# Performance work log

Hardware: AMD Instinct MI355X
Metric: run time of the kernel (lower is better)

The kernel has to match this reference:

```python
import jax, jax.numpy as jnp
import numpy as np

D_MODEL = 768
H = 12
D_FF = 3072
EPS = 1e-6


def _layernorm(x, alpha, bias):
    # torch.std default is Bessel-corrected (ddof=1); denom is (std + eps)
    mean = jnp.mean(x, axis=-1, keepdims=True)
    var = jnp.sum((x - mean) ** 2, axis=-1, keepdims=True) / (x.shape[-1] - 1)
    std = jnp.sqrt(var)
    return alpha * (x - mean) / (std + EPS) + bias


def _linear(x, w, b):
    # torch nn.Linear: y = x @ W.T + b, W is [out, in]
    return jnp.einsum('...i,oi->...o', x, w) + b


def setup_inputs() -> dict:
    key = jax.random.key(0)
    ks = jax.random.split(key, 16)
    B, S = 8, 1024
    sc = 1.0 / np.sqrt(D_MODEL)
    inp = {
        'x': jax.random.normal(ks[0], (B, S, D_MODEL), dtype=jnp.float32),
        'mask': jax.random.randint(ks[1], (B, 1, 1, S), 0, 2, dtype=jnp.int32),
        'wq': jax.random.normal(ks[2], (D_MODEL, D_MODEL), dtype=jnp.float32) * sc,
        'bq': jnp.zeros((D_MODEL,), jnp.float32),
        'wk': jax.random.normal(ks[3], (D_MODEL, D_MODEL), dtype=jnp.float32) * sc,
        'bk': jnp.zeros((D_MODEL,), jnp.float32),
        'wv': jax.random.normal(ks[4], (D_MODEL, D_MODEL), dtype=jnp.float32) * sc,
        'bv': jnp.zeros((D_MODEL,), jnp.float32),
        'wo': jax.random.normal(ks[5], (D_MODEL, D_MODEL), dtype=jnp.float32) * sc,
        'bo': jnp.zeros((D_MODEL,), jnp.float32),
        'ln1_a': jnp.ones((D_MODEL,), jnp.float32),
        'ln1_b': jnp.zeros((D_MODEL,), jnp.float32),
        'ln2_a': jnp.ones((D_MODEL,), jnp.float32),
        'ln2_b': jnp.zeros((D_MODEL,), jnp.float32),
        'w1': jax.random.normal(ks[6], (D_FF, D_MODEL), dtype=jnp.float32) * sc,
        'b1': jnp.zeros((D_FF,), jnp.float32),
        'w2': jax.random.normal(ks[7], (D_MODEL, D_FF), dtype=jnp.float32) * (1.0 / np.sqrt(D_FF)),
        'b2': jnp.zeros((D_MODEL,), jnp.float32),
    }
    return inp


def reference(x, mask, wq, bq, wk, bk, wv, bv, wo, bo,
              ln1_a, ln1_b, ln2_a, ln2_b, w1, b1, w2, b2):
    B, S, _ = x.shape
    d_k = D_MODEL // H

    # --- residual 1: pre-LN self-attention (dropout identity at eval) ---
    xn = _layernorm(x, ln1_a, ln1_b)
    q = _linear(xn, wq, bq).reshape(B, S, H, d_k).transpose(0, 2, 1, 3)
    k = _linear(xn, wk, bk).reshape(B, S, H, d_k).transpose(0, 2, 1, 3)
    v = _linear(xn, wv, bv).reshape(B, S, H, d_k).transpose(0, 2, 1, 3)

    scores = jnp.einsum('bhqd,bhkd->bhqk', q, k) / jnp.sqrt(jnp.float32(d_k))
    # faithful quirk: masked positions set to 1e-9, NOT -inf
    scores = jnp.where(mask == 0, jnp.float32(1e-9), scores)
    attn = jax.nn.softmax(scores, axis=-1)
    ctx = jnp.einsum('bhqk,bhkd->bhqd', attn, v)
    ctx = ctx.transpose(0, 2, 1, 3).reshape(B, S, D_MODEL)
    x = x + _linear(ctx, wo, bo)

    # --- residual 2: pre-LN feed-forward ---
    xn = _layernorm(x, ln2_a, ln2_b)
    ff = _linear(jax.nn.relu(_linear(xn, w1, b1)), w2, b2)
    return x + ff
```

## Files before the change

### kernel.cpp

```cpp
#include <hip/hip_runtime.h>
#include <stdint.h>

#define D_MODEL 768
#define D_FF    3072
#define NH      12
#define DK      64
#define BB      8
#define SS      1024
#define NTOK    (BB*SS)
#define QST     2304

typedef float          f32x4  __attribute__((ext_vector_type(4)));
typedef __bf16         bf16x8 __attribute__((ext_vector_type(8)));
typedef unsigned short us8v   __attribute__((ext_vector_type(8)));
typedef unsigned short us4v   __attribute__((ext_vector_type(4)));

__device__ __forceinline__ unsigned short f2b(float f) {
  unsigned int u = __builtin_bit_cast(unsigned int, f);
  u = (u + 0x7fffu + ((u >> 16) & 1u)) >> 16;
  return (unsigned short)u;
}
__device__ __forceinline__ float b2f(unsigned short h) {
  unsigned int u = ((unsigned int)h) << 16;
  return __builtin_bit_cast(float, u);
}
__device__ __forceinline__ float exp2a(float x) {
  float r; asm("v_exp_f32 %0, %1" : "=v"(r) : "v"(x)); return r;
}
__device__ __forceinline__ unsigned int cvtpk(float lo, float hi) {
  unsigned int r;
  asm("v_cvt_pk_bf16_f32 %0, %1, %2" : "=v"(r) : "v"(lo), "v"(hi));
  return r;
}

#define N4TOT 1769472
__global__ __launch_bounds__(256) void cast6_kernel(
    const float* __restrict__ s0, const float* __restrict__ s1,
    const float* __restrict__ s2, const float* __restrict__ s3,
    const float* __restrict__ s4, const float* __restrict__ s5,
    unsigned short* __restrict__ d0, unsigned short* __restrict__ d1,
    unsigned short* __restrict__ d2, unsigned short* __restrict__ d3,
    unsigned short* __restrict__ d4, unsigned short* __restrict__ d5) {
  int i = blockIdx.x * 256 + threadIdx.x;
  if (i >= N4TOT) return;
  const float* src; unsigned short* dst; int off;
  if (i < 147456)       { src = s0; dst = d0; off = i; }
  else if (i < 294912)  { src = s1; dst = d1; off = i - 147456; }
  else if (i < 442368)  { src = s2; dst = d2; off = i - 294912; }
  else if (i < 589824)  { src = s3; dst = d3; off = i - 442368; }
  else if (i < 1179648) { src = s4; dst = d4; off = i - 589824; }
  else                  { src = s5; dst = d5; off = i - 1179648; }
  float4 f = ((const float4*)src)[off];
  us4v o; o.x = f2b(f.x); o.y = f2b(f.y); o.z = f2b(f.z); o.w = f2b(f.w);
  *(us4v*)(dst + (size_t)off * 4) = o;
}

__global__ __launch_bounds__(256) void ln_kernel(const float* __restrict__ x,
                                                 const float* __restrict__ ga,
                                                 const float* __restrict__ gb,
                                                 unsigned short* __restrict__ y) {
  int row = blockIdx.x;
  const float* xr = x + (size_t)row * D_MODEL;
  int t = threadIdx.x, w = t >> 6, l = t & 63;
  float v0 = xr[t], v1 = xr[t + 256], v2 = xr[t + 512];
  float s = v0 + v1 + v2;
  #pragma unroll
  for (int off = 32; off; off >>= 1) s += __shfl_xor(s, off);
  __shared__ float red[4];
  __shared__ float stats[2];
  if (l == 0) red[w] = s;
  __syncthreads();
  if (t == 0) stats[0] = (red[0] + red[1] + red[2] + red[3]) * (1.0f / 768.0f);
  __syncthreads();
  float mean = stats[0];
  float d0 = v0 - mean, d1 = v1 - mean, d2 = v2 - mean;
  float ss = d0 * d0 + d1 * d1 + d2 * d2;
  #pragma unroll
  for (int off = 32; off; off >>= 1) ss += __shfl_xor(ss, off);
  __syncthreads();
  if (l == 0) red[w] = ss;
  __syncthreads();
  if (t == 0) {
    float tot = red[0] + red[1] + red[2] + red[3];
    stats[1] = 1.0f / (sqrtf(tot * (1.0f / 767.0f)) + 1e-6f);
  }
  __syncthreads();
  float inv = stats[1];
  unsigned short* yr = y + (size_t)row * D_MODEL;
  yr[t]       = f2b(ga[t]       * (d0 * inv) + gb[t]);
  yr[t + 256] = f2b(ga[t + 256] * (d1 * inv) + gb[t + 256]);
  yr[t + 512] = f2b(ga[t + 512] * (d2 * inv) + gb[t + 512]);
}

#define GLDS(g, l) __builtin_amdgcn_global_load_lds( \
    (__attribute__((address_space(1))) const void*)(g), \
    (__attribute__((address_space(3))) void*)(l), 16, 0, 0)

template<int BN>
__global__ __launch_bounds__(256) void gemm_t(
    const unsigned short* __restrict__ A,
    const unsigned short* __restrict__ W,
    const float* __restrict__ biasA,
    const float* __restrict__ biasB,
    const float* __restrict__ biasC,
    int segw,
    const float* __restrict__ resid,
    float* __restrict__ outF,
    unsigned short* __restrict__ outB,
    int M, int N, int K, int relu) {
  constexpr int BK  = (BN == 128) ? 32 : 64;
  constexpr int WC  = (BN == 128) ? 2 : 1;
  constexpr int MF  = (BN == 128) ? 4 : 2;
  constexpr int NF  = 4;
  constexpr int ASZ = 128 * BK;
  constexpr int BSZ = BN * BK;
  __shared__ unsigned short As[2 * ASZ];
  __shared__ unsigned short Bs[2 * BSZ];
  int t = threadIdx.x;
  int w = t >> 6, l = t & 63;
  int brow = blockIdx.x * 128;
  int bcol = blockIdx.y * BN;
  int wr = (w / WC) * (MF * 16);
  int wc = (w % WC) * (NF * 16);

  const unsigned short *ga0, *ga1, *gb0, *gb1;
  if constexpr (BN == 128) {
    ga0 = A + (size_t)(brow + (t >> 2)) * K + (t & 3) * 8;
    ga1 = ga0 + (size_t)64 * K;
    gb0 = W + (size_t)(bcol + (t >> 2)) * K + (t & 3) * 8;
    gb1 = gb0 + (size_t)64 * K;
  } else {
    int r5 = t >> 3;
    int swz = (t & 7) ^ (r5 & 7);
    ga0 = A + (size_t)(brow + r5) * K + swz * 8;
    gb0 = W + (size_t)(bcol + r5) * K + swz * 8;
    ga1 = gb1 = nullptr;
  }

  f32x4 acc[MF][NF];
  #pragma unroll
  for (int m = 0; m < MF; m++)
    #pragma unroll
    for (int n = 0; n < NF; n++)
      acc[m][n] = (f32x4){0.f, 0.f, 0.f, 0.f};

  int arow = wr + (l & 15);
  int bcw  = wc + (l & 15);
  int g    = l >> 4;
  int kk   = g * 8;
  const int nt = K / BK;

  auto stage = [&](int ti, int buf) {
    int k0 = ti * BK;
    if constexpr (BN == 128) {
      GLDS(ga0 + k0, As + buf * ASZ + t * 8);
      GLDS(ga1 + k0, As + buf * ASZ + 2048 + t * 8);
      GLDS(gb0 + k0, Bs + buf * BSZ + t * 8);
      GLDS(gb1 + k0, Bs + buf * BSZ + 2048 + t * 8);
    } else {
      #pragma unroll
      for (int i = 0; i < 4; i++)
        GLDS(ga0 + k0 + (size_t)(32 * i) * K, As + buf * ASZ + i * 2048 + t * 8);
      #pragma unroll
      for (int i = 0; i < 2; i++)
        GLDS(gb0 + k0 + (size_t)(32 * i) * K, Bs + buf * BSZ + i * 2048 + t * 8);
    }
  };

  stage(0, 0);
  __syncthreads();

  int cb = 0;
  for (int ti = 0; ti < nt; ti++) {
    if (ti + 1 < nt) stage(ti + 1, cb ^ 1);
    #pragma unroll
    for (int h = 0; h < BK / 32; h++) {
      bf16x8 af[MF], bfv[NF];
      #pragma unroll
      for (int m = 0; m < MF; m++) {
        int aro = arow + m * 16;
        if constexpr (BN == 128)
          af[m] = *(const bf16x8*)(As + cb * ASZ + aro * 32 + kk);
        else
          af[m] = *(const bf16x8*)(As + cb * ASZ + aro * 64 +
                                   ((((h << 2) + g) ^ (l & 7)) << 3));
      }
      #pragma unroll
      for (int n = 0; n < NF; n++) {
        int bco = bcw + n * 16;
        if constexpr (BN == 128)
          bfv[n] = *(const bf16x8*)(Bs + cb * BSZ + bco * 32 + kk);
        else
          bfv[n] = *(const bf16x8*)(Bs + cb * BSZ + bco * 64 +
                                    ((((h << 2) + g) ^ (l & 7)) << 3));
      }
      #pragma unroll
      for (int m = 0; m < MF; m++)
        #pragma unroll
        for (int n = 0; n < NF; n++)
          acc[m][n] = __builtin_amdgcn_mfma_f32_16x16x32_bf16(af[m], bfv[n], acc[m][n], 0, 0, 0);
    }
    if (ti + 1 < nt) __syncthreads();
    cb ^= 1;
  }

  #pragma unroll
  for (int n = 0; n < NF; n++) {
    int col = bcol + wc + n * 16 + (l & 15);
    int seg = col / segw, off = col - seg * segw;
    const float* bp = (seg == 0) ? biasA : ((seg == 1) ? biasB : biasC);
    float bv = bp[off];
    #pragma unroll
    for (int m = 0; m < MF; m++) {
      int row0 = brow + wr + m * 16 + (l >> 4) * 4;
      #pragma unroll
      for (int r = 0; r < 4; r++) {
        int row = row0 + r;
        float vacc = acc[m][n][r] + bv;
        if (resid) vacc += resid[(size_t)row * N + col];
        if (relu)  vacc = fmaxf(vacc, 0.f);
        if (outF)  outF[(size_t)row * N + col] = vacc;
        if (outB)  outB[(size_t)row * N + col] = f2b(vacc);
      }
    }
  }
}

#define PPAD 72
#define KPAD 72
#define SM_C1 0.18033688011112043f
#define SM_C2 1.4426950408889634e-9f

__global__ __launch_bounds__(256) void attn_mfma(
    const unsigned short* __restrict__ qkv,
    const int* __restrict__ mask,
    unsigned short* __restrict__ ctx) {
  int bh = blockIdx.x;
  int qt = blockIdx.y;
  int b = bh / NH, h = bh % NH;
  int t = threadIdx.x, w = t >> 6, l = t & 63;
  int ql = l & 15, g = l >> 4;

  const unsigned short* kp = qkv + 768 + h * DK;
  const unsigned short* vp = qkv + 1536 + h * DK;

  __shared__ unsigned short Ks[2][4096];
  __shared__ unsigned short Vt[64 * KPAD];
  __shared__ unsigned short Ps[128 * PPAD];
  __shared__ float mk01[64];

  int srow = t >> 3;
  int sblk = t & 7;
  int sb0  = sblk ^ (srow & 7);
  int sb1  = sblk ^ ((srow + 32) & 7);

  bf16x8 qf[2][2];
  {
    const unsigned short* qp = qkv + h * DK;
    size_t row0 = (size_t)(b * SS + qt * 128 + w * 32 + ql);
    #pragma unroll
    for (int s = 0; s < 2; s++)
      #pragma unroll
      for (int ks = 0; ks < 2; ks++)
        qf[s][ks] = *(const bf16x8*)(qp + (row0 + s * 16) * QST + ks * 32 + g * 8);
  }

  {
    size_t tok0 = (size_t)(b * SS);
    GLDS(kp + (tok0 + srow) * QST + sb0 * 8, &Ks[0][t * 8]);
    GLDS(kp + (tok0 + srow + 32) * QST + sb1 * 8, &Ks[0][2048 + t * 8]);
  }
  us8v vA, vB;
  {
    const unsigned short* vs = vp + ((size_t)(b * SS) + l) * QST + w * 16;
    vA = *(const us8v*)vs;
    vB = *(const us8v*)(vs + 8);
  }
  float mkreg = mask[b * SS + (t & 63)] ? 1.0f : 0.0f;

  f32x4 acc_o[2][4];
  #pragma unroll
  for (int s = 0; s < 2; s++)
    #pragma unroll
    for (int nf = 0; nf < 4; nf++) acc_o[s][nf] = (f32x4){0.f, 0.f, 0.f, 0.f};
  float mrun[2] = {-INFINITY, -INFINITY};
  float lrun[2] = {0.f, 0.f};

  int cur = 0;
  for (int kt = 0; kt < 16; kt++) {
    #pragma unroll
    for (int j = 0; j < 8; j++) {
      Vt[(w * 16 + j)     * KPAD + l] = vA[j];
      Vt[(w * 16 + 8 + j) * KPAD + l] = vB[j];
    }
    if (t < 64) mk01[t] = mkreg;
    __syncthreads();

    if (kt + 1 < 16) {
      size_t tn = (size_t)(b * SS + (kt + 1) * 64);
      GLDS(kp + (tn + srow) * QST + sb0 * 8, &Ks[cur ^ 1][t * 8]);
      GLDS(kp + (tn + srow + 32) * QST + sb1 * 8, &Ks[cur ^ 1][2048 + t * 8]);
      const unsigned short* vs2 = vp + (tn + l) * QST + w * 16;
      vA = *(const us8v*)vs2;
      vB = *(const us8v*)(vs2 + 8);
      mkreg = mask[b * SS + (kt + 1) * 64 + (t & 63)] ? 1.0f : 0.0f;
    }

    f32x4 sa[2][4];
    #pragma unroll
    for (int s = 0; s < 2; s++)
      #pragma unroll
      for (int kf = 0; kf < 4; kf++) sa[s][kf] = (f32x4){0.f, 0.f, 0.f, 0.f};
    #pragma unroll
    for (int ks = 0; ks < 2; ks++) {
      bf16x8 kfr[4];
      #pragma unroll
      for (int kf = 0; kf < 4; kf++) {
        int row = kf * 16 + ql;
        kfr[kf] = *(const bf16x8*)(&Ks[cur][row * 64 + ((g + 4 * ks) ^ (ql & 7)) * 8]);
      }
      #pragma unroll
      for (int s = 0; s < 2; s++)
        #pragma unroll
        for (int kf = 0; kf < 4; kf++)
          sa[s][kf] = __builtin_amdgcn_mfma_f32_16x16x32_bf16(kfr[kf], qf[s][ks], sa[s][kf], 0, 0, 0);
    }

    float m01v[16];
    #pragma unroll
    for (int kf = 0; kf < 4; kf++)
      #pragma unroll
      for (int r = 0; r < 4; r++)
        m01v[kf * 4 + r] = mk01[kf * 16 + g * 4 + r];

    #pragma unroll
    for (int s = 0; s < 2; s++) {
      float pv[16];
      float tm = -INFINITY;
      #pragma unroll
      for (int kf = 0; kf < 4; kf++)
        #pragma unroll
        for (int r = 0; r < 4; r++) {
          float xm = sa[s][kf][r] * SM_C1 - SM_C2;
          float sc = fmaf(m01v[kf * 4 + r], xm, SM_C2);
          pv[kf * 4 + r] = sc;
          tm = fmaxf(tm, sc);
        }
      tm = fmaxf(tm, __shfl_xor(tm, 16));
      tm = fmaxf(tm, __shfl_xor(tm, 32));
      bool renorm = !__all(tm <= mrun[s] + 8.0f);
      if (renorm) {
        float mn = fmaxf(mrun[s], tm);
        float corr = exp2a(mrun[s] - mn);
        mrun[s] = mn;
        lrun[s] *= corr;
        float c0 = __shfl(corr, (l & 48) | (g * 4 + 0));
        float c1 = __shfl(corr, (l & 48) | (g * 4 + 1));
        float c2 = __shfl(corr, (l & 48) | (g * 4 + 2));
        float c3 = __shfl(corr, (l & 48) | (g * 4 + 3));
        #pragma unroll
        for (int nf = 0; nf < 4; nf++) {
          acc_o[s][nf][0] *= c0; acc_o[s][nf][1] *= c1;
          acc_o[s][nf][2] *= c2; acc_o[s][nf][3] *= c3;
        }
      }
      float rs = 0.f;
      #pragma unroll
      for (int i = 0; i < 16; i++) { pv[i] = exp2a(pv[i] - mrun[s]); rs += pv[i]; }
      rs += __shfl_xor(rs, 16);
      rs += __shfl_xor(rs, 32);
      lrun[s] += rs;

      int prow = w * 32 + s * 16 + ql;
      #pragma unroll
      for (int kf = 0; kf < 4; kf++) {
        uint2 pk;
        pk.x = cvtpk(pv[kf * 4 + 0], pv[kf * 4 + 1]);
        pk.y = cvtpk(pv[kf * 4 + 2], pv[kf * 4 + 3]);
        *(uint2*)(Ps + prow * PPAD + kf * 16 + g * 4) = pk;
      }
    }

    #pragma unroll
    for (int ks = 0; ks < 2; ks++) {
      bf16x8 vfr[4];
      #pragma unroll
      for (int nf = 0; nf < 4; nf++)
        vfr[nf] = *(const bf16x8*)(Vt + (ql + nf * 16) * KPAD + g * 8 + ks * 32);
      #pragma unroll
      for (int s = 0; s < 2; s++) {
        bf16x8 pa = *(const bf16x8*)(Ps + (w * 32 + s * 16 + ql) * PPAD + g * 8 + ks * 32);
        #pragma unroll
        for (int nf = 0; nf < 4; nf++)
          acc_o[s][nf] = __builtin_amdgcn_mfma_f32_16x16x32_bf16(pa, vfr[nf], acc_o[s][nf], 0, 0, 0);
      }
    }
    __syncthreads();
    cur ^= 1;
  }

  #pragma unroll
  for (int s = 0; s < 2; s++) {
    float li0 = 1.0f / __shfl(lrun[s], (l & 48) | (g * 4 + 0));
    float li1 = 1.0f / __shfl(lrun[s], (l & 48) | (g * 4 + 1));
    float li2 = 1.0f / __shfl(lrun[s], (l & 48) | (g * 4 + 2));
    float li3 = 1.0f / __shfl(lrun[s], (l & 48) | (g * 4 + 3));
    #pragma unroll
    for (int nf = 0; nf < 4; nf++) {
      #pragma unroll
      for (int r = 0; r < 4; r++) {
        float li = (r == 0) ? li0 : (r == 1) ? li1 : (r == 2) ? li2 : li3;
        int tok = b * SS + qt * 128 + w * 32 + s * 16 + g * 4 + r;
        ctx[(size_t)tok * D_MODEL + h * DK + nf * 16 + ql] = f2b(acc_o[s][nf][r] * li);
      }
    }
  }
}

extern "C" void kernel_launch(void* const* d_in, const int* in_sizes, int n_in,
                              void* d_out, int out_size, void* d_ws, size_t ws_size,
                              hipStream_t stream) {
  const float* x    = (const float*)d_in[0];
  const int*   mask = (const int*)d_in[1];
  const float* wq   = (const float*)d_in[2];
  const float* bq   = (const float*)d_in[3];
  const float* wk   = (const float*)d_in[4];
  const float* bk   = (const float*)d_in[5];
  const float* wv   = (const float*)d_in[6];
  const float* bv   = (const float*)d_in[7];
  const float* wo   = (const float*)d_in[8];
  const float* bo   = (const float*)d_in[9];
  const float* ln1a = (const float*)d_in[10];
  const float* ln1b = (const float*)d_in[11];
  const float* ln2a = (const float*)d_in[12];
  const float* ln2b = (const float*)d_in[13];
  const float* w1   = (const float*)d_in[14];
  const float* b1   = (const float*)d_in[15];
  const float* w2   = (const float*)d_in[16];
  const float* b2   = (const float*)d_in[17];

  char* ws = (char*)d_ws;
  unsigned short* wqkvb = (unsigned short*)(ws + 0);
  unsigned short* wob   = (unsigned short*)(ws + 3538944);
  unsigned short* w1b   = (unsigned short*)(ws + 4718592);
  unsigned short* w2b   = (unsigned short*)(ws + 9437184);
  unsigned short* xnb   = (unsigned short*)(ws + 14155776);
  unsigned short* qkvb  = (unsigned short*)(ws + 26738688);
  unsigned short* ctxb  = (unsigned short*)(ws + 64487424);
  float*          x1    = (float*)(ws + 26738688);
  unsigned short* h1b   = (unsigned short*)(ws + 51904512);

  cast6_kernel<<<N4TOT / 256, 256, 0, stream>>>(
      wq, wk, wv, wo, w1, w2,
      wqkvb, wqkvb + 589824, wqkvb + 1179648, wob, w1b, w2b);

  ln_kernel<<<NTOK, 256, 0, stream>>>(x, ln1a, ln1b, xnb);

  dim3 gqkv(NTOK / 128, QST / 128);
  gemm_t<128><<<gqkv, 256, 0, stream>>>(xnb, wqkvb, bq, bk, bv, 768,
                                        nullptr, nullptr, qkvb,
                                        NTOK, QST, D_MODEL, 0);

  dim3 ga(BB * NH, SS / 128);
  attn_mfma<<<ga, 256, 0, stream>>>(qkvb, mask, ctxb);

  dim3 gwo(NTOK / 128, D_MODEL / 64);
  gemm_t<64><<<gwo, 256, 0, stream>>>(ctxb, wob, bo, nullptr, nullptr, D_MODEL,
                                      x, x1, nullptr,
                                      NTOK, D_MODEL, D_MODEL, 0);

  ln_kernel<<<NTOK, 256, 0, stream>>>(x1, ln2a, ln2b, xnb);

  dim3 gff(NTOK / 128, D_FF / 128);
  gemm_t<128><<<gff, 256, 0, stream>>>(xnb, w1b, b1, nullptr, nullptr, D_FF,
                                       nullptr, nullptr, h1b,
                                       NTOK, D_FF, D_MODEL, 1);

  dim3 gff2(NTOK / 128, D_MODEL / 64);
  gemm_t<64><<<gff2, 256, 0, stream>>>(h1b, w2b, b2, nullptr, nullptr, D_MODEL,
                                       x1, (float*)d_out, nullptr,
                                       NTOK, D_MODEL, D_FF, 0);
}
```

Before: 283.8 us.

## Keep softmax probabilities in registers via permuted V layout; drop K double buffer

The P tile no longer goes through shared memory. V columns are stored in a permuted slot order so that each lane's own probability registers already form the MFMA A-operand, which removes the Ps LDS write/read round trip. The K double buffer and the register prefetch of the next V/mask tile are removed, so loads now happen inside the current iteration before the barrier and shared memory usage drops. s_setprio is raised around the MFMA phases. The catch is that global load latency is now exposed each iteration, offset only by the higher occupancy that the smaller LDS footprint allows.

Measured after the change: 293.2 us. 1.03x slower.

```diff
diff --git a/kernel.cpp b/kernel.cpp
--- a/kernel.cpp
+++ b/kernel.cpp
@@ -226,7 +226,6 @@
   }
 }
 
-#define PPAD 72
 #define KPAD 72
 #define SM_C1 0.18033688011112043f
 #define SM_C2 1.4426950408889634e-9f
@@ -244,15 +243,15 @@
   const unsigned short* kp = qkv + 768 + h * DK;
   const unsigned short* vp = qkv + 1536 + h * DK;
 
-  __shared__ unsigned short Ks[2][4096];
+  __shared__ unsigned short Ks[4096];
   __shared__ unsigned short Vt[64 * KPAD];
-  __shared__ unsigned short Ps[128 * PPAD];
   __shared__ float mk01[64];
 
   int srow = t >> 3;
   int sblk = t & 7;
   int sb0  = sblk ^ (srow & 7);
   int sb1  = sblk ^ ((srow + 32) & 7);
+  int slotl = (l & 32) | ((l & 12) << 1) | ((l & 16) >> 2) | (l & 3);
 
   bf16x8 qf[2][2];
   {
@@ -265,19 +264,6 @@
         qf[s][ks] = *(const bf16x8*)(qp + (row0 + s * 16) * QST + ks * 32 + g * 8);
   }
 
-  {
-    size_t tok0 = (size_t)(b * SS);
-    GLDS(kp + (tok0 + srow) * QST + sb0 * 8, &Ks[0][t * 8]);
-    GLDS(kp + (tok0 + srow + 32) * QST + sb1 * 8, &Ks[0][2048 + t * 8]);
-  }
-  us8v vA, vB;
-  {
-    const unsigned short* vs = vp + ((size_t)(b * SS) + l) * QST + w * 16;
-    vA = *(const us8v*)vs;
-    vB = *(const us8v*)(vs + 8);
-  }
-  float mkreg = mask[b * SS + (t & 63)] ? 1.0f : 0.0f;
-
   f32x4 acc_o[2][4];
   #pragma unroll
   for (int s = 0; s < 2; s++)
@@ -286,38 +272,36 @@
   float mrun[2] = {-INFINITY, -INFINITY};
   float lrun[2] = {0.f, 0.f};
 
-  int cur = 0;
   for (int kt = 0; kt < 16; kt++) {
-    #pragma unroll
-    for (int j = 0; j < 8; j++) {
-      Vt[(w * 16 + j)     * KPAD + l] = vA[j];
-      Vt[(w * 16 + 8 + j) * KPAD + l] = vB[j];
-    }
-    if (t < 64) mk01[t] = mkreg;
+    size_t tok0 = (size_t)(b * SS + kt * 64);
+    {
+      const unsigned short* vsrc = vp + (tok0 + l) * QST + w * 16;
+      us8v v0 = *(const us8v*)vsrc;
+      us8v v1 = *(const us8v*)(vsrc + 8);
+      GLDS(kp + (tok0 + srow)      * QST + sb0 * 8, Ks + t * 8);
+      GLDS(kp + (tok0 + srow + 32) * QST + sb1 * 8, Ks + 2048 + t * 8);
+      #pragma unroll
+      for (int j = 0; j < 8; j++) {
+        Vt[(w * 16 + j)     * KPAD + slotl] = v0[j];
+        Vt[(w * 16 + 8 + j) * KPAD + slotl] = v1[j];
+      }
+    }
+    if (t < 64) mk01[t] = mask[b * SS + kt * 64 + t] ? 1.0f : 0.0f;
     __syncthreads();
 
-    if (kt + 1 < 16) {
-      size_t tn = (size_t)(b * SS + (kt + 1) * 64);
-      GLDS(kp + (tn + srow) * QST + sb0 * 8, &Ks[cur ^ 1][t * 8]);
-      GLDS(kp + (tn + srow + 32) * QST + sb1 * 8, &Ks[cur ^ 1][2048 + t * 8]);
-      const unsigned short* vs2 = vp + (tn + l) * QST + w * 16;
-      vA = *(const us8v*)vs2;
-      vB = *(const us8v*)(vs2 + 8);
-      mkreg = mask[b * SS + (kt + 1) * 64 + (t & 63)] ? 1.0f : 0.0f;
-    }
-
     f32x4 sa[2][4];
     #pragma unroll
     for (int s = 0; s < 2; s++)
       #pragma unroll
       for (int kf = 0; kf < 4; kf++) sa[s][kf] = (f32x4){0.f, 0.f, 0.f, 0.f};
+    __builtin_amdgcn_s_setprio(1);
     #pragma unroll
     for (int ks = 0; ks < 2; ks++) {
       bf16x8 kfr[4];
       #pragma unroll
       for (int kf = 0; kf < 4; kf++) {
         int row = kf * 16 + ql;
-        kfr[kf] = *(const bf16x8*)(&Ks[cur][row * 64 + ((g + 4 * ks) ^ (ql & 7)) * 8]);
+        kfr[kf] = *(const bf16x8*)(Ks + row * 64 + ((g + 4 * ks) ^ (ql & 7)) * 8);
       }
       #pragma unroll
       for (int s = 0; s < 2; s++)
@@ -325,6 +309,7 @@
         for (int kf = 0; kf < 4; kf++)
           sa[s][kf] = __builtin_amdgcn_mfma_f32_16x16x32_bf16(kfr[kf], qf[s][ks], sa[s][kf], 0, 0, 0);
     }
+    __builtin_amdgcn_s_setprio(0);
 
     float m01v[16];
     #pragma unroll
@@ -333,6 +318,7 @@
       for (int r = 0; r < 4; r++)
         m01v[kf * 4 + r] = mk01[kf * 16 + g * 4 + r];
 
+    uint4 paw[2][2];
     #pragma unroll
     for (int s = 0; s < 2; s++) {
       float pv[16];
@@ -371,16 +357,16 @@
       rs += __shfl_xor(rs, 32);
       lrun[s] += rs;
 
-      int prow = w * 32 + s * 16 + ql;
-      #pragma unroll
-      for (int kf = 0; kf < 4; kf++) {
-        uint2 pk;
-        pk.x = cvtpk(pv[kf * 4 + 0], pv[kf * 4 + 1]);
-        pk.y = cvtpk(pv[kf * 4 + 2], pv[kf * 4 + 3]);
-        *(uint2*)(Ps + prow * PPAD + kf * 16 + g * 4) = pk;
-      }
-    }
-
+      #pragma unroll
+      for (int ks = 0; ks < 2; ks++) {
+        paw[s][ks].x = cvtpk(pv[8 * ks + 0], pv[8 * ks + 1]);
+        paw[s][ks].y = cvtpk(pv[8 * ks + 2], pv[8 * ks + 3]);
+        paw[s][ks].z = cvtpk(pv[8 * ks + 4], pv[8 * ks + 5]);
+        paw[s][ks].w = cvtpk(pv[8 * ks + 6], pv[8 * ks + 7]);
+      }
+    }
+
+    __builtin_amdgcn_s_setprio(1);
     #pragma unroll
     for (int ks = 0; ks < 2; ks++) {
       bf16x8 vfr[4];
@@ -389,14 +375,14 @@
         vfr[nf] = *(const bf16x8*)(Vt + (ql + nf * 16) * KPAD + g * 8 + ks * 32);
       #pragma unroll
       for (int s = 0; s < 2; s++) {
-        bf16x8 pa = *(const bf16x8*)(Ps + (w * 32 + s * 16 + ql) * PPAD + g * 8 + ks * 32);
+        bf16x8 pa = __builtin_bit_cast(bf16x8, paw[s][ks]);
         #pragma unroll
         for (int nf = 0; nf < 4; nf++)
           acc_o[s][nf] = __builtin_amdgcn_mfma_f32_16x16x32_bf16(pa, vfr[nf], acc_o[s][nf], 0, 0, 0);
       }
     }
+    __builtin_amdgcn_s_setprio(0);
     __syncthreads();
-    cur ^= 1;
   }
 
   #pragma unroll
```
